# Optimization experiments

Hardware: AMD Instinct MI355X
Metric: run time of the kernel (lower is better)

## Reference

```python
import jax, jax.numpy as jnp
import numpy as np

NUM_HEADS = 16
DIM_K = 128
DIM_V = 128
ROPE_BASE = 10000.0


def rope(x):
    # x: [..., seq, d]; rotate-half convention
    d = x.shape[-1]
    seq = x.shape[-2]
    half = d // 2
    inv_freq = 1.0 / (ROPE_BASE ** (jnp.arange(0, half, dtype=jnp.float32) / half))
    ang = jnp.arange(seq, dtype=jnp.float32)[:, None] * inv_freq[None, :]  # [seq, half]
    cos, sin = jnp.cos(ang), jnp.sin(ang)
    x1, x2 = x[..., :half], x[..., half:]
    return jnp.concatenate([x1 * cos - x2 * sin, x1 * sin + x2 * cos], axis=-1)


def setup_inputs() -> dict:
    key = jax.random.key(0)
    ks = jax.random.split(key, 8)
    B, S, D = 2, 2048, 2048
    s = lambda fan_in: 1.0 / np.sqrt(fan_in)
    return {
        'q_in': jax.random.normal(ks[0], (B, S, D), jnp.float32),
        'k_in': jax.random.normal(ks[1], (B, S, D), jnp.float32),
        'v_in': jax.random.normal(ks[2], (B, S, D), jnp.float32),
        'mask': jnp.zeros((B, S), dtype=bool),
        'Wq': jax.random.normal(ks[3], (D, NUM_HEADS * DIM_K), jnp.float32) * s(D),
        'bq': jnp.zeros((NUM_HEADS * DIM_K,), jnp.float32),
        'Wk': jax.random.normal(ks[4], (D, DIM_K), jnp.float32) * s(D),
        'bk': jnp.zeros((DIM_K,), jnp.float32),
        'Wv': jax.random.normal(ks[5], (D, DIM_V), jnp.float32) * s(D),
        'bv': jnp.zeros((DIM_V,), jnp.float32),
        'Wo': jax.random.normal(ks[6], (NUM_HEADS * DIM_V, D), jnp.float32) * s(NUM_HEADS * DIM_V),
        'bo': jnp.zeros((D,), jnp.float32),
    }


def reference(q_in, k_in, v_in, mask, Wq, bq, Wk, bk, Wv, bv, Wo, bo):
    B, Sq, _ = q_in.shape
    Sk = k_in.shape[1]
    # projections: multi-head Q, single shared K/V head (MQA)
    q = (q_in @ Wq + bq).reshape(B, Sq, NUM_HEADS, DIM_K).transpose(0, 2, 1, 3)  # [B,H,Sq,dk]
    k = k_in @ Wk + bk  # [B,Sk,dk]
    v = v_in @ Wv + bv  # [B,Sk,dv]
    # inline RoPE on q and k
    q = rope(q)
    k = rope(k)
    scores = jnp.einsum('bhqd,bkd->bhqk', q, k) / np.sqrt(DIM_K)  # [B,H,Sq,Sk]
    # padding mask: True means masked out
    scores = jnp.where(mask[:, None, None, :], -jnp.inf, scores)
    # causal mask
    causal = jnp.triu(jnp.ones((Sq, Sk), dtype=bool), k=1)
    scores = jnp.where(causal[None, None], -jnp.inf, scores)
    weights = jax.nn.softmax(scores, axis=-1)
    attn = jnp.einsum('bhqk,bkd->bhqd', weights, v)  # [B,H,Sq,dv]
    attn = attn.transpose(0, 2, 1, 3).reshape(B, Sq, NUM_HEADS * DIM_V)
    return attn @ Wo + bo
```

## Files before the change

### kernel.cpp

```cpp
#include <hip/hip_runtime.h>

#define NHEADS 16
#define DKV 128
#define BB 2
#define SS 2048
#define DD 2048

typedef __attribute__((ext_vector_type(8))) short bf16x8;
typedef __attribute__((ext_vector_type(4))) short bf16x4;
typedef __attribute__((ext_vector_type(4))) float f32x4;
typedef __attribute__((ext_vector_type(8))) _Float16 f16x8;

#define QSCL 0.12752775f

__device__ __forceinline__ short f2bf(float x) {
  unsigned u = __builtin_bit_cast(unsigned, x);
  unsigned r = (u + 0x7fffu + ((u >> 16) & 1u)) >> 16;
  return (short)(unsigned short)r;
}
__device__ __forceinline__ float bf2f(short s) {
  unsigned u = ((unsigned)(unsigned short)s) << 16;
  return __builtin_bit_cast(float, u);
}
__device__ __forceinline__ unsigned pk2bf(float a, float b) {
#if __has_builtin(__builtin_amdgcn_cvt_pk_bf16_f32)
  typedef __attribute__((ext_vector_type(2))) __bf16 bf2_t;
  bf2_t r = __builtin_amdgcn_cvt_pk_bf16_f32(a, b);
  return __builtin_bit_cast(unsigned, r);
#else
  unsigned ua = __builtin_bit_cast(unsigned, a);
  unsigned ub = __builtin_bit_cast(unsigned, b);
  return ((ua + 0x8000u) >> 16) | ((ub + 0x8000u) & 0xffff0000u);
#endif
}
__device__ __forceinline__ unsigned pkf16(float a, float b) {
#if __has_builtin(__builtin_amdgcn_cvt_pkrtz)
  typedef __attribute__((ext_vector_type(2))) __fp16 h2_t;
  h2_t r = __builtin_amdgcn_cvt_pkrtz(a, b);
  return __builtin_bit_cast(unsigned, r);
#else
  _Float16 ha = (_Float16)a, hb = (_Float16)b;
  unsigned short ua = __builtin_bit_cast(unsigned short, ha);
  unsigned short ub = __builtin_bit_cast(unsigned short, hb);
  return (unsigned)ua | ((unsigned)ub << 16);
#endif
}
__device__ __forceinline__ float exp2fast(float x) {
#if __has_builtin(__builtin_amdgcn_exp2f)
  return __builtin_amdgcn_exp2f(x);
#else
  return exp2f(x);
#endif
}

__device__ __forceinline__ void async16(const void* g, void* l) {
  __builtin_amdgcn_global_load_lds(
      (__attribute__((address_space(1))) void*)g,
      (__attribute__((address_space(3))) void*)l, 16, 0, 0);
}

__global__ __launch_bounds__(256) void cvt_q(const float* __restrict__ x,
                                             short* __restrict__ y) {
  int idx = blockIdx.x * 256 + threadIdx.x;
  int g = idx * 8;
  float4 a = *(const float4*)(x + g);
  float4 b = *(const float4*)(x + g + 4);
  uint4 o = {pk2bf(a.x, a.y), pk2bf(a.z, a.w), pk2bf(b.x, b.y), pk2bf(b.z, b.w)};
  *(uint4*)(y + g) = o;
}

__global__ __launch_bounds__(256) void transpose_w(
    const float* __restrict__ W, short* __restrict__ Wt, int K, int N,
    float scale) {
  __shared__ float T[32][33];
  const int nt = blockIdx.x * 32;
  const int kt = blockIdx.y * 32;
  const int tx = threadIdx.x & 31;
  const int ty = threadIdx.x >> 5;
#pragma unroll
  for (int i = 0; i < 4; ++i)
    T[ty + i * 8][tx] = W[(size_t)(kt + ty + i * 8) * N + nt + tx];
  __syncthreads();
#pragma unroll
  for (int i = 0; i < 4; ++i)
    Wt[(size_t)(nt + ty + i * 8) * K + kt + tx] = f2bf(T[tx][ty + i * 8] * scale);
}

__global__ void mask_bias(const unsigned char* __restrict__ m,
                          float* __restrict__ mb) {
  int i = blockIdx.x * 256 + threadIdx.x;
  mb[i] = m[i] ? -1e30f : 0.0f;
}

template <int AMODE>
__global__ __launch_bounds__(256) void gemm_as(
    const void* __restrict__ Ap, const short* __restrict__ Bt,
    const float* __restrict__ bias, void* __restrict__ Cp,
    int M, int N, int K, int KC, int cmode, float bscale) {
  __shared__ __align__(16) short As[128 * 32];
  __shared__ __align__(16) short Bs[128 * 32];
  const int tid = threadIdx.x;
  const int bm = blockIdx.y * 128;
  const int bn = blockIdx.x * 128;
  const int kz = blockIdx.z;
  const int w = tid >> 6, lane = tid & 63;
  const int lm = lane & 15, q4 = lane >> 4;
  const int m0 = (w & 1) * 64, n0 = (w >> 1) * 64;

  f32x4 acc[4][4];
#pragma unroll
  for (int mi = 0; mi < 4; ++mi)
#pragma unroll
    for (int ni = 0; ni < 4; ++ni) acc[mi][ni] = (f32x4){0.f, 0.f, 0.f, 0.f};

  const int kbeg = kz * KC;
  const int kend = kbeg + KC;

  for (int k0 = kbeg; k0 < kend; k0 += 32) {
    __syncthreads();
    if (AMODE == 1) {
      const short* Ab = (const short*)Ap;
#pragma unroll
      for (int i = 0; i < 2; ++i) {
        int rA = (w * 2 + i) * 16 + (lane >> 2);
        int cA = (lane & 3) ^ (rA & 3);
        async16(Ab + (size_t)(bm + rA) * K + k0 + cA * 8, &As[(w * 2 + i) * 512]);
      }
    } else {
      const float* Af = (const float*)Ap;
      float4 av[4];
#pragma unroll
      for (int i = 0; i < 4; ++i) {
        int qd = tid + i * 256;
        int r = qd >> 3, cq = qd & 7;
        av[i] = *(const float4*)(Af + (size_t)(bm + r) * K + k0 + cq * 4);
      }
#pragma unroll
      for (int i = 0; i < 4; ++i) {
        int qd = tid + i * 256;
        int r = qd >> 3, cq = qd & 7;
        int ch = cq >> 1, hf = cq & 1;
        int pc = ch ^ (r & 3);
        bf16x4 t = {f2bf(av[i].x), f2bf(av[i].y), f2bf(av[i].z), f2bf(av[i].w)};
        *(bf16x4*)&As[r * 32 + pc * 8 + hf * 4] = t;
      }
    }
#pragma unroll
    for (int i = 0; i < 2; ++i) {
      int rB = (w * 2 + i) * 16 + (lane >> 2);
      int cB = (lane & 3) ^ (rB & 3);
      async16(Bt + (size_t)(bn + rB) * K + k0 + cB * 8, &Bs[(w * 2 + i) * 512]);
    }
    __syncthreads();

    bf16x8 af[4], bf[4];
#pragma unroll
    for (int mi = 0; mi < 4; ++mi)
      af[mi] = *(const bf16x8*)&As[(m0 + mi * 16 + lm) * 32 + ((q4 ^ (lm & 3)) * 8)];
#pragma unroll
    for (int ni = 0; ni < 4; ++ni)
      bf[ni] = *(const bf16x8*)&Bs[(n0 + ni * 16 + lm) * 32 + ((q4 ^ (lm & 3)) * 8)];
#pragma unroll
    for (int mi = 0; mi < 4; ++mi)
#pragma unroll
      for (int ni = 0; ni < 4; ++ni)
        acc[mi][ni] = __builtin_amdgcn_mfma_f32_16x16x32_bf16(
            af[mi], bf[ni], acc[mi][ni], 0, 0, 0);
  }

  if (cmode == 2) {
    float* Cf = (float*)Cp + (size_t)kz * M * N;
#pragma unroll
    for (int mi = 0; mi < 4; ++mi)
#pragma unroll
      for (int ni = 0; ni < 4; ++ni)
#pragma unroll
        for (int reg = 0; reg < 4; ++reg)
          Cf[(size_t)(bm + m0 + mi * 16 + q4 * 4 + reg) * N +
             (bn + n0 + ni * 16 + lm)] = acc[mi][ni][reg];
  } else {
#pragma unroll
    for (int mi = 0; mi < 4; ++mi)
#pragma unroll
      for (int ni = 0; ni < 4; ++ni)
#pragma unroll
        for (int reg = 0; reg < 4; ++reg) {
          int rowg = bm + m0 + mi * 16 + q4 * 4 + reg;
          int colg = bn + n0 + ni * 16 + lm;
          float val = acc[mi][ni][reg] + bias[colg] * bscale;
          if (cmode == 0)
            ((float*)Cp)[(size_t)rowg * N + colg] = val;
          else
            ((short*)Cp)[(size_t)rowg * N + colg] = f2bf(val);
        }
  }
}

#define SPLITK 4
__global__ __launch_bounds__(256) void kv_reduce(
    const float* __restrict__ kpart, const float* __restrict__ vpart,
    const float* __restrict__ bk, const float* __restrict__ bv,
    short* __restrict__ kp, short* __restrict__ vtb) {
  __shared__ float Kt[32][128];
  __shared__ short Vl[128][36];
  const int tid = threadIdx.x;
  const int r0 = blockIdx.x * 32;
#pragma unroll
  for (int i = 0; i < 16; ++i) {
    int e = tid + i * 256;
    int r = e >> 7, c = e & 127;
    float sk = 0.f, sv = 0.f;
#pragma unroll
    for (int z = 0; z < SPLITK; ++z) {
      sk += kpart[((size_t)z * 4096 + r0 + r) * 128 + c];
      sv += vpart[((size_t)z * 4096 + r0 + r) * 128 + c];
    }
    Kt[r][c] = sk + bk[c];
    Vl[c][r] = f2bf(sv + bv[c]);
  }
  __syncthreads();
#pragma unroll
  for (int i = 0; i < 8; ++i) {
    int e = tid + i * 256;
    int r = e >> 6, d = e & 63;
    float x1 = Kt[r][d], x2 = Kt[r][d + 64];
    float s = (float)((r0 + r) & (SS - 1));
    float ang = s * exp2fast((float)d * (-13.287712379549449f / 64.0f));
    float sn, cs;
    __sincosf(ang, &sn, &cs);
    kp[(size_t)(r0 + r) * 128 + d] = f2bf(x1 * cs - x2 * sn);
    kp[(size_t)(r0 + r) * 128 + d + 64] = f2bf(x1 * sn + x2 * cs);
  }
  const int b = r0 >> 11;
  const int j = tid >> 1, soff = (tid & 1) * 16;
  short* dst = vtb + ((size_t)b * 128 + j) * SS + (r0 & (SS - 1)) + soff;
#pragma unroll
  for (int t = 0; t < 2; ++t) {
    bf16x8 tmp;
#pragma unroll
    for (int u = 0; u < 8; ++u) tmp[u] = Vl[j][soff + t * 8 + u];
    *(bf16x8*)(dst + t * 8) = tmp;
  }
}

__global__ __launch_bounds__(256) void rope_q(short* __restrict__ qp) {
  int idx = blockIdx.x * 256 + threadIdx.x;
  int j8 = idx & 7;
  int h = (idx >> 3) & (NHEADS - 1);
  int s = (idx >> 7) & (SS - 1);
  int b = idx >> 18;
  short* base = qp + (((size_t)b * SS + s) * NHEADS + h) * DKV + j8 * 8;
  bf16x8 x1 = *(bf16x8*)base;
  bf16x8 x2 = *(bf16x8*)(base + 64);
  bf16x8 y1, y2;
#pragma unroll
  for (int j = 0; j < 8; ++j) {
    int d = j8 * 8 + j;
    float ang = (float)s * exp2fast((float)d * (-13.287712379549449f / 64.0f));
    float sn, cs;
    __sincosf(ang, &sn, &cs);
    float a = bf2f(x1[j]), bb2 = bf2f(x2[j]);
    y1[j] = f2bf(a * cs - bb2 * sn);
    y2[j] = f2bf(a * sn + bb2 * cs);
  }
  *(bf16x8*)base = y1;
  *(bf16x8*)(base + 64) = y2;
}

#define PSTR 40

__global__ __launch_bounds__(512, 4) void flash_kernel(
    const short* __restrict__ q, const short* __restrict__ k,
    const short* __restrict__ vt, const float* __restrict__ mb,
    short* __restrict__ out, short* __restrict__ pO, float* __restrict__ pL) {
  __shared__ __align__(16) short Kb[2][32 * 128];
  __shared__ __align__(16) short Vb[2][128 * 64];
  __shared__ __align__(16) short Ps[8][16 * PSTR];
  const int j = blockIdx.x;
  const int cls = j >> 5, hb = j & 31;
  int qx, c;
  if (cls < 8) {
    qx = cls + 8; c = 0;
  } else {
    int kk = (cls - 8) >> 1;
    if ((cls & 1) == 0) { qx = 15 - kk; c = 1; }
    else                { qx = 7 - kk;  c = 0; }
  }
  const int h = hb & 15, b = hb >> 4;
  const int kt0 = c ? 32 : 0;
  int kend = 4 * qx + 4;
  if (c == 0 && kend > 32) kend = 32;

  const int tid = threadIdx.x;
  const int w = tid >> 6, lane = tid & 63;
  const int lm = lane & 15, q4 = lane >> 4;
  const int qrow0 = qx * 128 + w * 16;

  bf16x8 qf[4];
#pragma unroll
  for (int ks = 0; ks < 4; ++ks)
    qf[ks] = *(const bf16x8*)(q +
        ((size_t)b * SS + qrow0 + lm) * (NHEADS * DKV) + h * DKV +
        ks * 32 + q4 * 8);

  bf16x8 onesb;
#pragma unroll
  for (int jj = 0; jj < 8; ++jj) onesb[jj] = (short)0x3F80;

  f32x4 O[8], Ol;
#pragma unroll
  for (int vi = 0; vi < 8; ++vi) O[vi] = (f32x4){0.f, 0.f, 0.f, 0.f};
  Ol = (f32x4){0.f, 0.f, 0.f, 0.f};

  const size_t kbase = (size_t)b * SS;

  {
    {
      int r = w * 4 + (lane >> 4);
      int cc = (lane & 15) ^ (r & 7);
      async16(k + (kbase + (size_t)kt0 * 32 + r) * DKV + cc * 8,
              &Kb[0][w * 512]);
    }
#pragma unroll
    for (int i = 0; i < 2; ++i) {
      int rV = (w * 2 + i) * 8 + (lane >> 3);
      int cV = (lane & 7) ^ (rV & 7);
      async16(vt + ((size_t)b * DKV + rV) * SS + (size_t)kt0 * 32 + cV * 8,
              &Vb[0][(w * 2 + i) * 512]);
    }
  }
  f32x4 mc0 = *(const f32x4*)(mb + kbase + (size_t)kt0 * 32 + q4 * 4);
  f32x4 mc1 = *(const f32x4*)(mb + kbase + (size_t)kt0 * 32 + 16 + q4 * 4);

  for (int kt = kt0; kt < kend; ++kt) {
    __syncthreads();

    f32x4 mn0, mn1;
    if (kt + 1 < kend) {
      const int t = kt + 1;
      {
        int r = w * 4 + (lane >> 4);
        int cc = (lane & 15) ^ (r & 7);
        async16(k + (kbase + (size_t)t * 32 + r) * DKV + cc * 8,
                &Kb[t & 1][w * 512]);
      }
      if (kt & 1) {
#pragma unroll
        for (int i = 0; i < 2; ++i) {
          int rV = (w * 2 + i) * 8 + (lane >> 3);
          int cV = (lane & 7) ^ (rV & 7);
          async16(vt + ((size_t)b * DKV + rV) * SS + (size_t)t * 32 + cV * 8,
                  &Vb[(t >> 1) & 1][(w * 2 + i) * 512]);
        }
      }
      mn0 = *(const f32x4*)(mb + kbase + (size_t)t * 32 + q4 * 4);
      mn1 = *(const f32x4*)(mb + kbase + (size_t)t * 32 + 16 + q4 * 4);
    }

    const short* Kc = Kb[kt & 1];
    f32x4 sacc[2];
#pragma unroll
    for (int mi = 0; mi < 2; ++mi) sacc[mi] = (f32x4){0.f, 0.f, 0.f, 0.f};
#pragma unroll
    for (int mi = 0; mi < 2; ++mi)
#pragma unroll
      for (int ks = 0; ks < 4; ++ks) {
        bf16x8 kf = *(const bf16x8*)&Kc[(mi * 16 + lm) * 128 +
                                        (((ks * 4 + q4) ^ (lm & 7)) << 3)];
        sacc[mi] = __builtin_amdgcn_mfma_f32_16x16x32_bf16(
            kf, qf[ks], sacc[mi], 0, 0, 0);
      }

    const bool diag = (kt >= 4 * qx);
#pragma unroll
    for (int mi = 0; mi < 2; ++mi) {
      f32x4 mbv = mi ? mc1 : mc0;
      float pv[4];
#pragma unroll
      for (int reg = 0; reg < 4; ++reg) {
        float s = sacc[mi][reg] + mbv[reg];
        if (diag) {
          int kg = kt * 32 + mi * 16 + q4 * 4 + reg;
          int qg = qrow0 + lm;
          if (kg > qg) s = -1e30f;
        }
        pv[reg] = exp2fast(s);
      }
      uint2 pkd = {pk2bf(pv[0], pv[1]), pk2bf(pv[2], pv[3])};
      *(uint2*)&Ps[w][lm * PSTR + mi * 16 + q4 * 4] = pkd;
    }
    mc0 = mn0;
    mc1 = mn1;

    const short* Vc = Vb[(kt >> 1) & 1];
    const int hf4 = (kt & 1) * 4;
    bf16x8 pf = *(const bf16x8*)&Ps[w][lm * PSTR + q4 * 8];
    Ol = __builtin_amdgcn_mfma_f32_16x16x32_bf16(pf, onesb, Ol, 0, 0, 0);
#pragma unroll
    for (int vi = 0; vi < 8; ++vi) {
      bf16x8 vf = *(const bf16x8*)&Vc[(vi * 16 + lm) * 64 +
                                      (((hf4 + q4) ^ (lm & 7)) << 3)];
      O[vi] = __builtin_amdgcn_mfma_f32_16x16x32_bf16(pf, vf, O[vi], 0, 0, 0);
    }
  }

  __syncthreads();
  float* Wr = (float*)&Vb[0][0] + w * 544;
  float linv[4];
#pragma unroll
  for (int reg = 0; reg < 4; ++reg) linv[reg] = 1.0f / Ol[reg];

  const bool split = (qx >= 8);
  short* obase;
  int ostr;
  if (split) {
    int slot = ((b * 16 + h) * 8 + (qx - 8)) * 2 + c;
    obase = pO + (size_t)slot * (128 * 128);
    ostr = 128;
    if (lm == 0) {
      float* dl = pL + (size_t)slot * 128 + w * 16;
#pragma unroll
      for (int reg = 0; reg < 4; ++reg)
        dl[q4 * 4 + reg] = Ol[reg];
    }
  } else {
    obase = out + ((size_t)b * SS + qx * 128) * (NHEADS * DKV) + h * DKV;
    ostr = NHEADS * DKV;
  }

#pragma unroll
  for (int qd = 0; qd < 4; ++qd) {
#pragma unroll
    for (int v2 = 0; v2 < 2; ++v2) {
      int vi = qd * 2 + v2;
#pragma unroll
      for (int reg = 0; reg < 4; ++reg)
        Wr[(q4 * 4 + reg) * 34 + v2 * 16 + lm] = O[vi][reg] * linv[reg];
    }
    int r = lane & 15, hh = lane >> 4;
    f32x4 t0 = *(const f32x4*)&Wr[r * 34 + hh * 8];
    f32x4 t1 = *(const f32x4*)&Wr[r * 34 + hh * 8 + 4];
    size_t oaddr = (size_t)(w * 16 + r) * ostr + qd * 32 + hh * 8;
    uint4 o0;
    if (split) {
      o0 = (uint4){pkf16(t0[0], t0[1]), pkf16(t0[2], t0[3]),
                   pkf16(t1[0], t1[1]), pkf16(t1[2], t1[3])};
    } else {
      o0 = (uint4){pk2bf(t0[0], t0[1]), pk2bf(t0[2], t0[3]),
                   pk2bf(t1[0], t1[1]), pk2bf(t1[2], t1[3])};
    }
    *(uint4*)(obase + oaddr) = o0;
  }
}

__global__ __launch_bounds__(256) void combine(
    const short* __restrict__ pO, const float* __restrict__ pL,
    short* __restrict__ out) {
  const int qxi = blockIdx.x, h = blockIdx.y, b = blockIdx.z;
  const int qx = 8 + qxi;
  const int slot2 = ((b * 16 + h) * 8 + qxi) * 2;
  const _Float16* p0 = (const _Float16*)(pO + (size_t)slot2 * (128 * 128));
  const _Float16* p1 = p0 + 128 * 128;
  const float* l0 = pL + (size_t)slot2 * 128;
  const float* l1 = l0 + 128;
  const int t = threadIdx.x;
  const int row = t >> 1, half = t & 1;
  const float w0 = l0[row], w1 = l1[row];
  const float inv = 1.0f / (w0 + w1);
  const float a0 = w0 * inv, a1 = w1 * inv;
  const int off = row * 128 + half * 64;
  short* dst = out + ((size_t)(b * SS + qx * 128 + row)) * (NHEADS * DKV) +
               h * DKV + half * 64;
#pragma unroll
  for (int v = 0; v < 8; ++v) {
    f16x8 x0 = *(const f16x8*)(p0 + off + v * 8);
    f16x8 x1 = *(const f16x8*)(p1 + off + v * 8);
    float r[8];
#pragma unroll
    for (int u = 0; u < 8; ++u)
      r[u] = (float)x0[u] * a0 + (float)x1[u] * a1;
    uint4 o = {pk2bf(r[0], r[1]), pk2bf(r[2], r[3]),
               pk2bf(r[4], r[5]), pk2bf(r[6], r[7])};
    *(uint4*)(dst + v * 8) = o;
  }
}

extern "C" void kernel_launch(void* const* d_in, const int* in_sizes, int n_in,
                              void* d_out, int out_size, void* d_ws, size_t ws_size,
                              hipStream_t stream) {
  const float* q_in = (const float*)d_in[0];
  const float* k_in = (const float*)d_in[1];
  const float* v_in = (const float*)d_in[2];
  const unsigned char* mask = (const unsigned char*)d_in[3];
  const float* Wq = (const float*)d_in[4];
  const float* bq = (const float*)d_in[5];
  const float* Wk = (const float*)d_in[6];
  const float* bk = (const float*)d_in[7];
  const float* Wv = (const float*)d_in[8];
  const float* bv = (const float*)d_in[9];
  const float* Wo = (const float*)d_in[10];
  const float* bo = (const float*)d_in[11];

  const int M = BB * SS;
  short* Wqt = (short*)d_ws;
  short* Wot = Wqt + (size_t)DD * DD;
  short* Wkt = Wot + (size_t)DD * DD;
  short* Wvt = Wkt + (size_t)DKV * DD;
  short* qb  = Wvt + (size_t)DKV * DD;
  short* qp  = qb + (size_t)M * DD;
  short* kp  = qp + (size_t)M * DD;
  short* vtb = kp + (size_t)M * DKV;
  float* mb  = (float*)(vtb + (size_t)BB * DKV * SS);
  float* kpart = mb + (size_t)BB * SS;
  float* vpart = kpart + (size_t)SPLITK * M * DKV;
  float* pL = vpart + (size_t)SPLITK * M * DKV;
  short* ap = qb;
  short* pO = (short*)kpart;

  cvt_q<<<M * DD / (8 * 256), 256, 0, stream>>>(q_in, qb);
  transpose_w<<<dim3(DD / 32, DD / 32), 256, 0, stream>>>(Wq, Wqt, DD, DD, QSCL);
  transpose_w<<<dim3(DKV / 32, DD / 32), 256, 0, stream>>>(Wk, Wkt, DD, DKV, 1.0f);
  transpose_w<<<dim3(DKV / 32, DD / 32), 256, 0, stream>>>(Wv, Wvt, DD, DKV, 1.0f);
  transpose_w<<<dim3(DD / 32, DD / 32), 256, 0, stream>>>(Wo, Wot, DD, DD, 1.0f);
  mask_bias<<<BB * SS / 256, 256, 0, stream>>>(mask, mb);

  gemm_as<1><<<dim3(DD / 128, M / 128, 1), 256, 0, stream>>>(
      qb, Wqt, bq, qp, M, DD, DD, DD, 1, QSCL);
  gemm_as<0><<<dim3(1, M / 128, SPLITK), 256, 0, stream>>>(
      k_in, Wkt, nullptr, kpart, M, DKV, DD, DD / SPLITK, 2, 1.0f);
  gemm_as<0><<<dim3(1, M / 128, SPLITK), 256, 0, stream>>>(
      v_in, Wvt, nullptr, vpart, M, DKV, DD, DD / SPLITK, 2, 1.0f);
  kv_reduce<<<M / 32, 256, 0, stream>>>(kpart, vpart, bk, bv, kp, vtb);
  rope_q<<<(BB * SS * NHEADS * 8) / 256, 256, 0, stream>>>(qp);

  flash_kernel<<<dim3(768), 512, 0, stream>>>(qp, kp, vtb, mb, ap, pO, pL);
  combine<<<dim3(8, NHEADS, BB), 256, 0, stream>>>(pO, pL, ap);

  gemm_as<1><<<dim3(DD / 128, M / 128, 1), 256, 0, stream>>>(
      ap, Wot, bo, d_out, M, DD, DD, DD, 0, 1.0f);
}
```

Before: 420.1 us.

## Fuse preprocessing kernels, merge K/V GEMMs, apply Q RoPE inside flash kernel

```diff
diff --git a/kernel.cpp b/kernel.cpp
--- a/kernel.cpp
+++ b/kernel.cpp
@@ -59,20 +59,14 @@
       (__attribute__((address_space(3))) void*)l, 16, 0, 0);
 }
 
-__global__ __launch_bounds__(256) void cvt_q(const float* __restrict__ x,
-                                             short* __restrict__ y) {
-  int idx = blockIdx.x * 256 + threadIdx.x;
-  int g = idx * 8;
-  float4 a = *(const float4*)(x + g);
-  float4 b = *(const float4*)(x + g + 4);
-  uint4 o = {pk2bf(a.x, a.y), pk2bf(a.z, a.w), pk2bf(b.x, b.y), pk2bf(b.z, b.w)};
-  *(uint4*)(y + g) = o;
-}
-
-__global__ __launch_bounds__(256) void transpose_w(
-    const float* __restrict__ W, short* __restrict__ Wt, int K, int N,
-    float scale) {
+__global__ __launch_bounds__(256) void transpose_w2(
+    const float* __restrict__ W0, short* __restrict__ Wt0,
+    const float* __restrict__ W1, short* __restrict__ Wt1,
+    int K, int N, float s0, float s1) {
   __shared__ float T[32][33];
+  const float* W = blockIdx.z ? W1 : W0;
+  short* Wt = blockIdx.z ? Wt1 : Wt0;
+  const float scale = blockIdx.z ? s1 : s0;
   const int nt = blockIdx.x * 32;
   const int kt = blockIdx.y * 32;
   const int tx = threadIdx.x & 31;
@@ -84,12 +78,6 @@
 #pragma unroll
   for (int i = 0; i < 4; ++i)
     Wt[(size_t)(nt + ty + i * 8) * K + kt + tx] = f2bf(T[tx][ty + i * 8] * scale);
-}
-
-__global__ void mask_bias(const unsigned char* __restrict__ m,
-                          float* __restrict__ mb) {
-  int i = blockIdx.x * 256 + threadIdx.x;
-  mb[i] = m[i] ? -1e30f : 0.0f;
 }
 
 template <int AMODE>
@@ -197,14 +185,96 @@
 }
 
 #define SPLITK 4
+__global__ __launch_bounds__(256) void gemm_kv(
+    const float* __restrict__ Ak, const float* __restrict__ Av,
+    const short* __restrict__ Btk, const short* __restrict__ Btv,
+    float* __restrict__ kpart, float* __restrict__ vpart) {
+  __shared__ __align__(16) short As[128 * 32];
+  __shared__ __align__(16) short Bs[128 * 32];
+  const int tid = threadIdx.x;
+  const int bm = blockIdx.y * 128;
+  const int z = blockIdx.z;
+  const int kz = z & 3;
+  const float* Af = (z >= 4) ? Av : Ak;
+  const short* Bt = (z >= 4) ? Btv : Btk;
+  float* Cf = ((z >= 4) ? vpart : kpart) + (size_t)kz * (4096 * 128);
+  const int K = DD, N = DKV;
+  const int w = tid >> 6, lane = tid & 63;
+  const int lm = lane & 15, q4 = lane >> 4;
+  const int m0 = (w & 1) * 64, n0 = (w >> 1) * 64;
+
+  f32x4 acc[4][4];
+#pragma unroll
+  for (int mi = 0; mi < 4; ++mi)
+#pragma unroll
+    for (int ni = 0; ni < 4; ++ni) acc[mi][ni] = (f32x4){0.f, 0.f, 0.f, 0.f};
+
+  const int kbeg = kz * (DD / SPLITK);
+  const int kend = kbeg + DD / SPLITK;
+
+  for (int k0 = kbeg; k0 < kend; k0 += 32) {
+    __syncthreads();
+    {
+      float4 av[4];
+#pragma unroll
+      for (int i = 0; i < 4; ++i) {
+        int qd = tid + i * 256;
+        int r = qd >> 3, cq = qd & 7;
+        av[i] = *(const float4*)(Af + (size_t)(bm + r) * K + k0 + cq * 4);
+      }
+#pragma unroll
+      for (int i = 0; i < 4; ++i) {
+        int qd = tid + i * 256;
+        int r = qd >> 3, cq = qd & 7;
+        int ch = cq >> 1, hf = cq & 1;
+        int pc = ch ^ (r & 3);
+        bf16x4 t = {f2bf(av[i].x), f2bf(av[i].y), f2bf(av[i].z), f2bf(av[i].w)};
+        *(bf16x4*)&As[r * 32 + pc * 8 + hf * 4] = t;
+      }
+    }
+#pragma unroll
+    for (int i = 0; i < 2; ++i) {
+      int rB = (w * 2 + i) * 16 + (lane >> 2);
+      int cB = (lane & 3) ^ (rB & 3);
+      async16(Bt + (size_t)rB * K + k0 + cB * 8, &Bs[(w * 2 + i) * 512]);
+    }
+    __syncthreads();
+
+    bf16x8 af[4], bf[4];
+#pragma unroll
+    for (int mi = 0; mi < 4; ++mi)
+      af[mi] = *(const bf16x8*)&As[(m0 + mi * 16 + lm) * 32 + ((q4 ^ (lm & 3)) * 8)];
+#pragma unroll
+    for (int ni = 0; ni < 4; ++ni)
+      bf[ni] = *(const bf16x8*)&Bs[(n0 + ni * 16 + lm) * 32 + ((q4 ^ (lm & 3)) * 8)];
+#pragma unroll
+    for (int mi = 0; mi < 4; ++mi)
+#pragma unroll
+      for (int ni = 0; ni < 4; ++ni)
+        acc[mi][ni] = __builtin_amdgcn_mfma_f32_16x16x32_bf16(
+            af[mi], bf[ni], acc[mi][ni], 0, 0, 0);
+  }
+
+#pragma unroll
+  for (int mi = 0; mi < 4; ++mi)
+#pragma unroll
+    for (int ni = 0; ni < 4; ++ni)
+#pragma unroll
+      for (int reg = 0; reg < 4; ++reg)
+        Cf[(size_t)(bm + m0 + mi * 16 + q4 * 4 + reg) * N +
+           (n0 + ni * 16 + lm)] = acc[mi][ni][reg];
+}
+
 __global__ __launch_bounds__(256) void kv_reduce(
     const float* __restrict__ kpart, const float* __restrict__ vpart,
     const float* __restrict__ bk, const float* __restrict__ bv,
-    short* __restrict__ kp, short* __restrict__ vtb) {
+    short* __restrict__ kp, short* __restrict__ vtb,
+    const unsigned char* __restrict__ m, float* __restrict__ mb) {
   __shared__ float Kt[32][128];
   __shared__ short Vl[128][36];
   const int tid = threadIdx.x;
   const int r0 = blockIdx.x * 32;
+  if (tid < 32) mb[r0 + tid] = m[r0 + tid] ? -1e30f : 0.0f;
 #pragma unroll
   for (int i = 0; i < 16; ++i) {
     int e = tid + i * 256;
@@ -241,30 +311,6 @@
     for (int u = 0; u < 8; ++u) tmp[u] = Vl[j][soff + t * 8 + u];
     *(bf16x8*)(dst + t * 8) = tmp;
   }
-}
-
-__global__ __launch_bounds__(256) void rope_q(short* __restrict__ qp) {
-  int idx = blockIdx.x * 256 + threadIdx.x;
-  int j8 = idx & 7;
-  int h = (idx >> 3) & (NHEADS - 1);
-  int s = (idx >> 7) & (SS - 1);
-  int b = idx >> 18;
-  short* base = qp + (((size_t)b * SS + s) * NHEADS + h) * DKV + j8 * 8;
-  bf16x8 x1 = *(bf16x8*)base;
-  bf16x8 x2 = *(bf16x8*)(base + 64);
-  bf16x8 y1, y2;
-#pragma unroll
-  for (int j = 0; j < 8; ++j) {
-    int d = j8 * 8 + j;
-    float ang = (float)s * exp2fast((float)d * (-13.287712379549449f / 64.0f));
-    float sn, cs;
-    __sincosf(ang, &sn, &cs);
-    float a = bf2f(x1[j]), bb2 = bf2f(x2[j]);
-    y1[j] = f2bf(a * cs - bb2 * sn);
-    y2[j] = f2bf(a * sn + bb2 * cs);
-  }
-  *(bf16x8*)base = y1;
-  *(bf16x8*)(base + 64) = y2;
 }
 
 #define PSTR 40
@@ -302,6 +348,26 @@
     qf[ks] = *(const bf16x8*)(q +
         ((size_t)b * SS + qrow0 + lm) * (NHEADS * DKV) + h * DKV +
         ks * 32 + q4 * 8);
+  {
+    float s = (float)(qrow0 + lm);
+#pragma unroll
+    for (int ks = 0; ks < 2; ++ks) {
+      bf16x8 x1 = qf[ks], x2 = qf[ks + 2];
+      bf16x8 y1, y2;
+#pragma unroll
+      for (int jj = 0; jj < 8; ++jj) {
+        int d = ks * 32 + q4 * 8 + jj;
+        float ang = s * exp2fast((float)d * (-13.287712379549449f / 64.0f));
+        float sn, cs;
+        __sincosf(ang, &sn, &cs);
+        float a = bf2f(x1[jj]), b2 = bf2f(x2[jj]);
+        y1[jj] = f2bf(a * cs - b2 * sn);
+        y2[jj] = f2bf(a * sn + b2 * cs);
+      }
+      qf[ks] = y1;
+      qf[ks + 2] = y2;
+    }
+  }
 
   bf16x8 onesb;
 #pragma unroll
@@ -517,21 +583,16 @@
   short* ap = qb;
   short* pO = (short*)kpart;
 
-  cvt_q<<<M * DD / (8 * 256), 256, 0, stream>>>(q_in, qb);
-  transpose_w<<<dim3(DD / 32, DD / 32), 256, 0, stream>>>(Wq, Wqt, DD, DD, QSCL);
-  transpose_w<<<dim3(DKV / 32, DD / 32), 256, 0, stream>>>(Wk, Wkt, DD, DKV, 1.0f);
-  transpose_w<<<dim3(DKV / 32, DD / 32), 256, 0, stream>>>(Wv, Wvt, DD, DKV, 1.0f);
-  transpose_w<<<dim3(DD / 32, DD / 32), 256, 0, stream>>>(Wo, Wot, DD, DD, 1.0f);
-  mask_bias<<<BB * SS / 256, 256, 0, stream>>>(mask, mb);
-
-  gemm_as<1><<<dim3(DD / 128, M / 128, 1), 256, 0, stream>>>(
-      qb, Wqt, bq, qp, M, DD, DD, DD, 1, QSCL);
-  gemm_as<0><<<dim3(1, M / 128, SPLITK), 256, 0, stream>>>(
-      k_in, Wkt, nullptr, kpart, M, DKV, DD, DD / SPLITK, 2, 1.0f);
-  gemm_as<0><<<dim3(1, M / 128, SPLITK), 256, 0, stream>>>(
-      v_in, Wvt, nullptr, vpart, M, DKV, DD, DD / SPLITK, 2, 1.0f);
-  kv_reduce<<<M / 32, 256, 0, stream>>>(kpart, vpart, bk, bv, kp, vtb);
-  rope_q<<<(BB * SS * NHEADS * 8) / 256, 256, 0, stream>>>(qp);
+  transpose_w2<<<dim3(DD / 32, DD / 32, 2), 256, 0, stream>>>(
+      Wq, Wqt, Wo, Wot, DD, DD, QSCL, 1.0f);
+  transpose_w2<<<dim3(DKV / 32, DD / 32, 2), 256, 0, stream>>>(
+      Wk, Wkt, Wv, Wvt, DD, DKV, 1.0f, 1.0f);
+
+  gemm_kv<<<dim3(1, M / 128, 2 * SPLITK), 256, 0, stream>>>(
+      k_in, v_in, Wkt, Wvt, kpart, vpart);
+  gemm_as<0><<<dim3(DD / 128, M / 128, 1), 256, 0, stream>>>(
+      q_in, Wqt, bq, qp, M, DD, DD, DD, 1, QSCL);
+  kv_reduce<<<M / 32, 256, 0, stream>>>(kpart, vpart, bk, bv, kp, vtb, mask, mb);
 
   flash_kernel<<<dim3(768), 512, 0, stream>>>(qp, kp, vtb, mb, ap, pO, pL);
   combine<<<dim3(8, NHEADS, BB), 256, 0, stream>>>(pO, pL, ap);
```

Measured after the change: 405.3 us. 1.04x faster.
